# Optimization experiments

Measured on AMD Instinct MI355X. Metric: run time of the kernel, lower is better.

Reference implementation:

```python
import jax, jax.numpy as jnp
import numpy as np

ALPHA = 0.2          # LeakyReLU negative slope
NEG_INF = -9e15      # mask value used by the torch module


def setup_inputs() -> dict:
    key = jax.random.key(0)
    k_x, k_adj, k_w, k_a = jax.random.split(key, 4)
    B, N, D, L = 8, 2048, 128, 3
    x = jax.random.normal(k_x, (B, N, D), dtype=jnp.float32)
    adj = jax.random.randint(k_adj, (B, N, N), 0, 2, dtype=jnp.int32)
    Wg = jax.random.normal(k_w, (L, D, D), dtype=jnp.float32) * 0.08  # ~Linear init scale
    bg = jnp.zeros((L, D), dtype=jnp.float32)
    attn_a = jax.random.normal(k_a, (L, 2 * D), dtype=jnp.float32) * 0.08
    return {"x": x, "adj": adj, "Wg": Wg, "bg": bg, "attn_a": attn_a}


def reference(x, adj, Wg, bg, attn_a):
    # x: [B,N,D], adj: [B,N,N] int, Wg: [L,D,D], bg: [L,D], attn_a: [L,2D]
    D = x.shape[-1]
    L = Wg.shape[0]
    mask = adj > 0
    for i in range(L):  # small fixed layer loop
        h = jax.nn.relu(x @ Wg[i] + bg[i])                       # [B,N,D]
        # a_input[b,i,j] = [h_i, h_j]; dot with a splits into two rank-1 terms,
        # avoiding the N*N*2D intermediate while computing identical math.
        s1 = h @ attn_a[i, :D]                                   # [B,N]
        s2 = h @ attn_a[i, D:]                                   # [B,N]
        e = jax.nn.leaky_relu(s1[:, :, None] + s2[:, None, :], ALPHA)  # [B,N,N]
        e = jnp.where(mask, e, NEG_INF)
        attn = jax.nn.softmax(e, axis=2)                         # masked softmax over neighbors
        # dropout p=0.0 -> identity
        x = x + jnp.einsum('bij,bjd->bid', attn, h)              # residual update
    return x
```

## Files before the change

kernel.cpp:

```cpp
#include <hip/hip_runtime.h>
#include <stdint.h>

typedef __attribute__((ext_vector_type(8))) short short8;
typedef __attribute__((ext_vector_type(4))) float f32x4;

__device__ __forceinline__ unsigned short f2bf(float f) {
    unsigned u = __float_as_uint(f);
    unsigned r = u + 0x7fffu + ((u >> 16) & 1u);
    return (unsigned short)(r >> 16);
}
__device__ __forceinline__ unsigned fenc(float f) {
    unsigned u = __float_as_uint(f);
    return (u & 0x80000000u) ? ~u : (u | 0x80000000u);
}
__device__ __forceinline__ float fdec(unsigned e) {
    unsigned u = (e & 0x80000000u) ? (e & 0x7fffffffu) : ~e;
    return __uint_as_float(u);
}

__global__ __launch_bounds__(256) void k_init(const float* __restrict__ xin,
                                              const float* __restrict__ Wf,
                                              float* __restrict__ xq,
                                              unsigned short* __restrict__ wTb,
                                              unsigned* __restrict__ s2mx) {
    int blk = blockIdx.x, tid = threadIdx.x;
    if (blk < 2048) {
        int e0 = (blk * 256 + tid) * 4;
        *(f32x4*)(xq + e0) = *(const f32x4*)(xin + e0);
    } else if (blk < 2240) {
        int c = (blk - 2048) * 256 + tid;
        int l = c >> 14, rem = c & 16383, n = rem >> 7, k = rem & 127;
        wTb[c] = f2bf(Wf[l * 16384 + k * 128 + n]);
    } else if (tid < 24) {
        s2mx[tid] = fenc(-3e38f);
    }
}

__global__ __launch_bounds__(256) void k_pack(const int* __restrict__ adj,
                                              unsigned long long* __restrict__ packed) {
    int w = (blockIdx.x * 256 + threadIdx.x) >> 6;
    int lane = threadIdx.x & 63;
    for (int k = 0; k < 64; k++) {
        int q = w * 64 + k;
        int row = q >> 5, wd = q & 31;
        int v = adj[row * 2048 + wd * 64 + lane];
        unsigned long long m = __ballot(v > 0);
        if (lane == 0) packed[q] = m;
    }
}

__global__ __launch_bounds__(256) void k_h(
    const float* __restrict__ xq, const unsigned short* __restrict__ wTb,
    const float* __restrict__ bF, const float* __restrict__ aF, int layer,
    unsigned short* __restrict__ hT, float* __restrict__ s1g,
    float* __restrict__ s2g, unsigned* __restrict__ s2mx)
{
    __shared__ short xs[64 * 136];
    __shared__ short wsb[128 * 136];
    __shared__ float s2blk[4];
    int blk = blockIdx.x, tid = threadIdx.x;
    int row0 = blk * 64, b = blk >> 5;
    int w = tid >> 6, lane = tid & 63, quad = lane >> 4, l15 = lane & 15;

    for (int c = tid; c < 1024; c += 256) {
        int r = c >> 4, kg = c & 15;
        const float* src = &xq[(row0 + r) * 128 + kg * 8];
        f32x4 v0 = *(const f32x4*)src;
        f32x4 v1 = *(const f32x4*)(src + 4);
        short8 o;
        o[0] = (short)f2bf(v0[0]); o[1] = (short)f2bf(v0[1]);
        o[2] = (short)f2bf(v0[2]); o[3] = (short)f2bf(v0[3]);
        o[4] = (short)f2bf(v1[0]); o[5] = (short)f2bf(v1[1]);
        o[6] = (short)f2bf(v1[2]); o[7] = (short)f2bf(v1[3]);
        *(short8*)&xs[r * 136 + kg * 8] = o;
    }
    const unsigned short* wl = wTb + layer * 16384;
    for (int c = tid; c < 2048; c += 256) {
        int n = c >> 4, kg = c & 15;
        *(short8*)&wsb[n * 136 + kg * 8] = *(const short8*)&wl[n * 128 + kg * 8];
    }
    __syncthreads();

    f32x4 acc[8];
#pragma unroll
    for (int t = 0; t < 8; t++) acc[t] = {0.f, 0.f, 0.f, 0.f};
#pragma unroll
    for (int ks = 0; ks < 4; ks++) {
        short8 af = *(const short8*)&xs[(w * 16 + l15) * 136 + ks * 32 + quad * 8];
#pragma unroll
        for (int t = 0; t < 8; t++) {
            short8 bf = *(const short8*)&wsb[(t * 16 + l15) * 136 + ks * 32 + quad * 8];
            acc[t] = __builtin_amdgcn_mfma_f32_16x16x32_bf16(af, bf, acc[t], 0, 0, 0);
        }
    }

    float s1p[4] = {0.f, 0.f, 0.f, 0.f}, s2p[4] = {0.f, 0.f, 0.f, 0.f};
#pragma unroll
    for (int t = 0; t < 8; t++) {
        int colg = t * 16 + l15;
        float bgf = bF[layer * 128 + colg];
        float a1 = aF[layer * 256 + colg];
        float a2 = aF[layer * 256 + 128 + colg];
#pragma unroll
        for (int r = 0; r < 4; r++) {
            float v = acc[t][r] + bgf;
            v = v > 0.f ? v : 0.f;
            acc[t][r] = v;
            s1p[r] = fmaf(v, a1, s1p[r]);
            s2p[r] = fmaf(v, a2, s2p[r]);
        }
    }
#pragma unroll
    for (int r = 0; r < 4; r++) {
#pragma unroll
        for (int off = 1; off < 16; off <<= 1) {
            s1p[r] += __shfl_xor(s1p[r], off, 64);
            s2p[r] += __shfl_xor(s2p[r], off, 64);
        }
    }
    if (l15 == 0) {
#pragma unroll
        for (int r = 0; r < 4; r++) {
            int rowg = row0 + w * 16 + quad * 4 + r;
            s1g[rowg] = s1p[r];
            s2g[rowg] = s2p[r];
        }
    }
    float mx = fmaxf(fmaxf(s2p[0], s2p[1]), fmaxf(s2p[2], s2p[3]));
    mx = fmaxf(mx, __shfl_xor(mx, 16, 64));
    mx = fmaxf(mx, __shfl_xor(mx, 32, 64));
    if (lane == 0) s2blk[w] = mx;
    __syncthreads();

    short* st = (short*)wsb;
#pragma unroll
    for (int t = 0; t < 8; t++)
#pragma unroll
        for (int r = 0; r < 4; r++)
            st[(w * 16 + quad * 4 + r) * 130 + t * 16 + l15] = (short)f2bf(acc[t][r]);
    __syncthreads();
    if (tid == 0) {
        float m2 = fmaxf(fmaxf(s2blk[0], s2blk[1]), fmaxf(s2blk[2], s2blk[3]));
        atomicMax(&s2mx[layer * 8 + b], fenc(m2));
    }
    int i0 = (blk & 31) * 64;
    for (int c = tid; c < 1024; c += 256) {
        int d = c >> 3, ig = c & 7;
        short8 o;
#pragma unroll
        for (int ii = 0; ii < 8; ii++) o[ii] = st[(ig * 8 + ii) * 130 + d];
        *(short8*)&hT[(b * 128 + d) * 2048 + i0 + ig * 8] = o;
    }
}

__global__ __launch_bounds__(512) void k_attn(
    const unsigned long long* __restrict__ packed,
    const unsigned short* __restrict__ hT, const float* __restrict__ s1g,
    const float* __restrict__ s2g, const unsigned* __restrict__ s2mx,
    int layer, float* __restrict__ xq)
{
    __shared__ short ht[2][144 * 72];
    __shared__ unsigned long long bits[64 * 32];
    int blk = blockIdx.x, tid = threadIdx.x;
    int b = blk >> 5;
    int rowg0 = blk * 64;
    int w = tid >> 6, lane = tid & 63, quad = lane >> 4, l15 = lane & 15;
    int wrow = w & 3, wj = w >> 2;

    for (int c = tid; c < 2048; c += 512) bits[c] = packed[rowg0 * 32 + c];
    for (int c = tid; c < 256; c += 512) {
        int tile = c >= 128;
        int cc = c - tile * 128;
        int d = 128 + (cc >> 3), jg = cc & 7;
        short8 v;
        short one = (short)0x3F80;
        if (d == 128) { v[0]=one;v[1]=one;v[2]=one;v[3]=one;v[4]=one;v[5]=one;v[6]=one;v[7]=one; }
        else { v[0]=0;v[1]=0;v[2]=0;v[3]=0;v[4]=0;v[5]=0;v[6]=0;v[7]=0; }
        *(short8*)&ht[tile][d * 72 + jg * 8] = v;
    }

    int rowA = wrow * 16 + l15;
    float s1v = s1g[rowg0 + rowA];
    float s2m = fdec(s2mx[layer * 8 + b]);
    float tmh = s1v + s2m;
    float mhat = fmaxf(tmh, 0.2f * tmh);
    f32x4 acc[9];
#pragma unroll
    for (int t = 0; t < 9; t++) acc[t] = {0.f, 0.f, 0.f, 0.f};

    int sc[4], sd[4], sjg[4];
#pragma unroll
    for (int s = 0; s < 4; s++) {
        int c = tid + 512 * s;
        sc[s] = c >> 10;
        int cc = c & 1023;
        sd[s] = cc >> 3; sjg[s] = cc & 7;
    }
    short8 pv[4];
#pragma unroll
    for (int s = 0; s < 4; s++) {
        int jts = sc[s] ? 16 : 0;
        pv[s] = *(const short8*)&hT[(b * 128 + sd[s]) * 2048 + jts * 64 + sjg[s] * 8];
    }

    const float* s2b = s2g + b * 2048;
    for (int it = 0; it < 16; it++) {
#pragma unroll
        for (int s = 0; s < 4; s++)
            *(short8*)&ht[sc[s]][sd[s] * 72 + sjg[s] * 8] = pv[s];
        __syncthreads();
        if (it < 15) {
#pragma unroll
            for (int s = 0; s < 4; s++) {
                int jts = (sc[s] ? 16 : 0) + it + 1;
                pv[s] = *(const short8*)&hT[(b * 128 + sd[s]) * 2048 + jts * 64 + sjg[s] * 8];
            }
        }
        int jt = wj * 16 + it;
        unsigned long long word = bits[rowA * 32 + jt];
#pragma unroll
        for (int ks = 0; ks < 2; ks++) {
            unsigned b8 = (unsigned)(word >> (ks * 32 + quad * 8)) & 0xffu;
            int jbase = jt * 64 + ks * 32 + quad * 8;
            f32x4 sa = *(const f32x4*)&s2b[jbase];
            f32x4 sb = *(const f32x4*)&s2b[jbase + 4];
            float sv[8] = {sa[0], sa[1], sa[2], sa[3], sb[0], sb[1], sb[2], sb[3]};
            short8 af;
#pragma unroll
            for (int jj = 0; jj < 8; jj++) {
                float e = s1v + sv[jj];
                e = fmaxf(e, 0.2f * e);
                float pvv = __expf(e - mhat);
                pvv = (b8 & (1u << jj)) ? pvv : 0.f;
                af[jj] = (short)f2bf(pvv);
            }
#pragma unroll
            for (int t = 0; t < 9; t++) {
                short8 bf = *(const short8*)&ht[wj][(t * 16 + l15) * 72 + ks * 32 + quad * 8];
                acc[t] = __builtin_amdgcn_mfma_f32_16x16x32_bf16(af, bf, acc[t], 0, 0, 0);
            }
        }
        __syncthreads();
    }

    float* red = (float*)&ht[0][0];
    if (wj == 1) {
#pragma unroll
        for (int t = 0; t < 9; t++)
#pragma unroll
            for (int r = 0; r < 4; r++)
                red[wrow * 16 * 148 + (quad * 4 + r) * 148 + t * 16 + l15] = acc[t][r];
    }
    __syncthreads();
    if (wj == 0) {
#pragma unroll
        for (int t = 0; t < 9; t++)
#pragma unroll
            for (int r = 0; r < 4; r++)
                acc[t][r] += red[wrow * 16 * 148 + (quad * 4 + r) * 148 + t * 16 + l15];
#pragma unroll
        for (int r = 0; r < 4; r++) {
            int rowgC = rowg0 + wrow * 16 + quad * 4 + r;
            float psum = __shfl(acc[8][r], lane & 48, 64);
            float rl = psum > 0.f ? 1.0f / psum : 0.f;
#pragma unroll
            for (int t = 0; t < 8; t++) {
                int idx = rowgC * 128 + t * 16 + l15;
                xq[idx] += acc[t][r] * rl;
            }
        }
    }
}

extern "C" void kernel_launch(void* const* d_in, const int* in_sizes, int n_in,
                              void* d_out, int out_size, void* d_ws, size_t ws_size,
                              hipStream_t stream) {
    const void* px = d_in[0];
    int ia = 1; long amax = -1;
    for (int i = 1; i < n_in; i++)
        if ((long)in_sizes[i] > amax) { amax = in_sizes[i]; ia = i; }
    int rem[8]; int m = 0;
    for (int i = 1; i < n_in && m < 8; i++) if (i != ia) rem[m++] = i;
    for (int i = 0; i < m; i++)
        for (int j = i + 1; j < m; j++)
            if (in_sizes[rem[j]] > in_sizes[rem[i]]) { int t = rem[i]; rem[i] = rem[j]; rem[j] = t; }
    const int*   padj = (const int*)((n_in > 1) ? d_in[ia] : d_in[0]);
    const float* pW = (const float*)((m > 0) ? d_in[rem[0]] : d_in[0]);
    const float* pa = (const float*)((m > 1) ? d_in[rem[1]] : d_in[0]);
    const float* pb = (const float*)((m > 2) ? d_in[rem[2]] : d_in[0]);

    float* xq = (float*)d_out;
    char* ws = (char*)d_ws;
    unsigned long long* packed = (unsigned long long*)ws;
    unsigned short* hT = (unsigned short*)(ws + 4194304);
    float* s1 = (float*)(ws + 8388608);
    float* s2 = (float*)(ws + 8454144);
    unsigned* s2mx = (unsigned*)(ws + 8519680);
    unsigned short* wTb = (unsigned short*)(ws + 8519808);

    k_init<<<2241, 256, 0, stream>>>((const float*)px, pW, xq, wTb, s2mx);
    k_pack<<<2048, 256, 0, stream>>>(padj, packed);
    for (int l = 0; l < 3; l++) {
        k_h<<<256, 256, 0, stream>>>(xq, wTb, pb, pa, l, hT, s1, s2, s2mx);
        k_attn<<<256, 512, 0, stream>>>(packed, hT, s1, s2, s2mx, l, xq);
    }
}
```

Measured before the change: 364.7 us.

## Split attention j-range across separate blocks with partial-sum combine kernel

Replaces the intra-block split of the neighbor (j) range across two wave groups with a split across two separate 256-thread blocks, doubling the grid to 512 blocks. Each block writes unnormalized partial outputs and row sums to workspace, and a new combine kernel adds the halves, normalizes, and applies the residual update. This aims to spread work over more CUs and drop the in-block LDS reduction. In exchange it adds a kernel launch per layer and extra global traffic for the partial outputs.

After: 368.5 us. Within noise of the previous version (+1.0%).

```diff
diff --git a/kernel.cpp b/kernel.cpp
--- a/kernel.cpp
+++ b/kernel.cpp
@@ -153,33 +153,31 @@
     }
 }
 
-__global__ __launch_bounds__(512) void k_attn(
+__global__ __launch_bounds__(256) void k_attn(
     const unsigned long long* __restrict__ packed,
     const unsigned short* __restrict__ hT, const float* __restrict__ s1g,
     const float* __restrict__ s2g, const unsigned* __restrict__ s2mx,
-    int layer, float* __restrict__ xq)
+    int layer, float* __restrict__ Opart, float* __restrict__ Ppart)
 {
-    __shared__ short ht[2][144 * 72];
+    __shared__ short ht[144 * 72];
     __shared__ unsigned long long bits[64 * 32];
     int blk = blockIdx.x, tid = threadIdx.x;
-    int b = blk >> 5;
-    int rowg0 = blk * 64;
+    int half = blk & 1, brow = blk >> 1;
+    int b = brow >> 5;
+    int rowg0 = brow * 64;
     int w = tid >> 6, lane = tid & 63, quad = lane >> 4, l15 = lane & 15;
-    int wrow = w & 3, wj = w >> 2;
-
-    for (int c = tid; c < 2048; c += 512) bits[c] = packed[rowg0 * 32 + c];
-    for (int c = tid; c < 256; c += 512) {
-        int tile = c >= 128;
-        int cc = c - tile * 128;
-        int d = 128 + (cc >> 3), jg = cc & 7;
+
+    for (int c = tid; c < 2048; c += 256) bits[c] = packed[rowg0 * 32 + c];
+    for (int c = tid; c < 128; c += 256) {
+        int d = 128 + (c >> 3), jg = c & 7;
         short8 v;
         short one = (short)0x3F80;
         if (d == 128) { v[0]=one;v[1]=one;v[2]=one;v[3]=one;v[4]=one;v[5]=one;v[6]=one;v[7]=one; }
         else { v[0]=0;v[1]=0;v[2]=0;v[3]=0;v[4]=0;v[5]=0;v[6]=0;v[7]=0; }
-        *(short8*)&ht[tile][d * 72 + jg * 8] = v;
-    }
-
-    int rowA = wrow * 16 + l15;
+        *(short8*)&ht[d * 72 + jg * 8] = v;
+    }
+
+    int rowA = w * 16 + l15;
     float s1v = s1g[rowg0 + rowA];
     float s2m = fdec(s2mx[layer * 8 + b]);
     float tmh = s1v + s2m;
@@ -188,18 +186,16 @@
 #pragma unroll
     for (int t = 0; t < 9; t++) acc[t] = {0.f, 0.f, 0.f, 0.f};
 
-    int sc[4], sd[4], sjg[4];
+    int sd[4], sjg[4];
 #pragma unroll
     for (int s = 0; s < 4; s++) {
-        int c = tid + 512 * s;
-        sc[s] = c >> 10;
-        int cc = c & 1023;
-        sd[s] = cc >> 3; sjg[s] = cc & 7;
+        int c = tid + 256 * s;
+        sd[s] = c >> 3; sjg[s] = c & 7;
     }
     short8 pv[4];
 #pragma unroll
     for (int s = 0; s < 4; s++) {
-        int jts = sc[s] ? 16 : 0;
+        int jts = half * 16;
         pv[s] = *(const short8*)&hT[(b * 128 + sd[s]) * 2048 + jts * 64 + sjg[s] * 8];
     }
 
@@ -207,16 +203,16 @@
     for (int it = 0; it < 16; it++) {
 #pragma unroll
         for (int s = 0; s < 4; s++)
-            *(short8*)&ht[sc[s]][sd[s] * 72 + sjg[s] * 8] = pv[s];
+            *(short8*)&ht[sd[s] * 72 + sjg[s] * 8] = pv[s];
         __syncthreads();
         if (it < 15) {
 #pragma unroll
             for (int s = 0; s < 4; s++) {
-                int jts = (sc[s] ? 16 : 0) + it + 1;
+                int jts = half * 16 + it + 1;
                 pv[s] = *(const short8*)&hT[(b * 128 + sd[s]) * 2048 + jts * 64 + sjg[s] * 8];
             }
         }
-        int jt = wj * 16 + it;
+        int jt = half * 16 + it;
         unsigned long long word = bits[rowA * 32 + jt];
 #pragma unroll
         for (int ks = 0; ks < 2; ks++) {
@@ -236,40 +232,38 @@
             }
 #pragma unroll
             for (int t = 0; t < 9; t++) {
-                short8 bf = *(const short8*)&ht[wj][(t * 16 + l15) * 72 + ks * 32 + quad * 8];
+                short8 bf = *(const short8*)&ht[(t * 16 + l15) * 72 + ks * 32 + quad * 8];
                 acc[t] = __builtin_amdgcn_mfma_f32_16x16x32_bf16(af, bf, acc[t], 0, 0, 0);
             }
         }
         __syncthreads();
     }
 
-    float* red = (float*)&ht[0][0];
-    if (wj == 1) {
-#pragma unroll
-        for (int t = 0; t < 9; t++)
-#pragma unroll
-            for (int r = 0; r < 4; r++)
-                red[wrow * 16 * 148 + (quad * 4 + r) * 148 + t * 16 + l15] = acc[t][r];
-    }
-    __syncthreads();
-    if (wj == 0) {
-#pragma unroll
-        for (int t = 0; t < 9; t++)
-#pragma unroll
-            for (int r = 0; r < 4; r++)
-                acc[t][r] += red[wrow * 16 * 148 + (quad * 4 + r) * 148 + t * 16 + l15];
-#pragma unroll
-        for (int r = 0; r < 4; r++) {
-            int rowgC = rowg0 + wrow * 16 + quad * 4 + r;
-            float psum = __shfl(acc[8][r], lane & 48, 64);
-            float rl = psum > 0.f ? 1.0f / psum : 0.f;
-#pragma unroll
-            for (int t = 0; t < 8; t++) {
-                int idx = rowgC * 128 + t * 16 + l15;
-                xq[idx] += acc[t][r] * rl;
-            }
-        }
-    }
+#pragma unroll
+    for (int r = 0; r < 4; r++) {
+        int rowgC = rowg0 + w * 16 + quad * 4 + r;
+        float psum = __shfl(acc[8][r], lane & 48, 64);
+        if (l15 == 0) Ppart[half * 16384 + rowgC] = psum;
+#pragma unroll
+        for (int t = 0; t < 8; t++)
+            Opart[((size_t)half * 16384 + rowgC) * 128 + t * 16 + l15] = acc[t][r];
+    }
+}
+
+__global__ __launch_bounds__(256) void k_comb(
+    const float* __restrict__ Opart, const float* __restrict__ Ppart,
+    float* __restrict__ xq)
+{
+    int idx = blockIdx.x * 256 + threadIdx.x;
+    int row = idx >> 5;
+    float p = Ppart[row] + Ppart[16384 + row];
+    float rl = p > 0.f ? 1.0f / p : 0.f;
+    f32x4 o0 = *(const f32x4*)&Opart[(size_t)idx * 4];
+    f32x4 o1 = *(const f32x4*)&Opart[(size_t)idx * 4 + 2097152];
+    f32x4 xv = *(const f32x4*)&xq[idx * 4];
+#pragma unroll
+    for (int k = 0; k < 4; k++) xv[k] += (o0[k] + o1[k]) * rl;
+    *(f32x4*)&xq[idx * 4] = xv;
 }
 
 extern "C" void kernel_launch(void* const* d_in, const int* in_sizes, int n_in,
@@ -297,11 +291,14 @@
     float* s2 = (float*)(ws + 8454144);
     unsigned* s2mx = (unsigned*)(ws + 8519680);
     unsigned short* wTb = (unsigned short*)(ws + 8519808);
+    float* Opart = (float*)(ws + 16777216);
+    float* Ppart = (float*)(ws + 33554432);
 
     k_init<<<2241, 256, 0, stream>>>((const float*)px, pW, xq, wTb, s2mx);
     k_pack<<<2048, 256, 0, stream>>>(padj, packed);
     for (int l = 0; l < 3; l++) {
         k_h<<<256, 256, 0, stream>>>(xq, wTb, pb, pa, l, hT, s1, s2, s2mx);
-        k_attn<<<256, 512, 0, stream>>>(packed, hT, s1, s2, s2mx, l, xq);
-    }
-}
+        k_attn<<<512, 256, 0, stream>>>(packed, hT, s1, s2, s2mx, l, Opart, Ppart);
+        k_comb<<<2048, 256, 0, stream>>>(Opart, Ppart, xq);
+    }
+}
```
